# Optimization experiments

Measured on AMD Instinct MI355X. Metric: run time of the kernel, lower is better.

## Reference

```python
import jax, jax.numpy as jnp
import numpy as np

HID = 50  # HIDDEN_SIZE in source


def _lstm_step(x, h, c, W_ih, W_hh, b):
    # PyTorch LSTM cell: gates order i, f, g, o
    gates = x @ W_ih.T + h @ W_hh.T + b  # [B, 4H]
    i, f, g, o = jnp.split(gates, 4, axis=-1)
    i = jax.nn.sigmoid(i)
    f = jax.nn.sigmoid(f)
    g = jnp.tanh(g)
    o = jax.nn.sigmoid(o)
    c = f * c + i * g
    h = o * jnp.tanh(c)
    return h, c


def setup_inputs() -> dict:
    key = jax.random.key(0)
    ks = jax.random.split(key, 11)
    B, S = 2048, 512
    H, I, O = HID, 1, 1
    s = 1.0 / np.sqrt(H)
    u = lambda k, shp: jax.random.uniform(k, shp, jnp.float32, -s, s)
    return {
        "source": jax.random.normal(ks[0], (B, S, I), jnp.float32),
        "enc_W_ih": u(ks[1], (4 * H, I)),
        "enc_W_hh": u(ks[2], (4 * H, H)),
        "enc_b_ih": u(ks[3], (4 * H,)),
        "enc_b_hh": u(ks[4], (4 * H,)),
        "dec_W_ih": u(ks[5], (4 * H, O)),
        "dec_W_hh": u(ks[6], (4 * H, H)),
        "dec_b_ih": u(ks[7], (4 * H,)),
        "dec_b_hh": u(ks[8], (4 * H,)),
        "fc_W": u(ks[9], (O, H)),
        "fc_b": u(ks[10], (O,)),
        "target_len": 256,
    }


def reference(source, enc_W_ih, enc_W_hh, enc_b_ih, enc_b_hh,
              dec_W_ih, dec_W_hh, dec_b_ih, dec_b_hh, fc_W, fc_b,
              target_len):
    B = source.shape[0]
    H = enc_W_hh.shape[1]
    dt = source.dtype
    h0 = jnp.zeros((B, H), dt)
    c0 = jnp.zeros((B, H), dt)

    enc_b = enc_b_ih + enc_b_hh

    def enc_step(carry, x_t):
        h, c = carry
        h, c = _lstm_step(x_t, h, c, enc_W_ih, enc_W_hh, enc_b)
        return (h, c), None

    # scan over time: [S, B, 1]
    (h, c), _ = jax.lax.scan(enc_step, (h0, c0), jnp.swapaxes(source, 0, 1))

    dec_b = dec_b_ih + dec_b_hh
    x0 = jnp.zeros((B, source.shape[2]), dt)  # decoder_input = zeros

    def dec_step(carry, _):
        x, h, c = carry
        h, c = _lstm_step(x, h, c, dec_W_ih, dec_W_hh, dec_b)
        y = h @ fc_W.T + fc_b  # [B, 1]
        return (y, h, c), y  # feed output back as next input

    _, ys = jax.lax.scan(dec_step, (x0, h, c), None, length=target_len)
    return jnp.swapaxes(ys, 0, 1)  # [B, target_len, 1]
```

## Files before the change

### kernel.cpp

```cpp
#include <hip/hip_runtime.h>


#define HID 50
#define SEQ 512
#define TGT 256
#define MB  4
#define L2E 1.44269504088896341f

typedef __attribute__((ext_vector_type(8))) short short8;
typedef __attribute__((ext_vector_type(4))) float f32x4;

__device__ __forceinline__ unsigned short f2bf(float f) {
    unsigned u = __float_as_uint(f);
    return (unsigned short)((u + 0x7fffu + ((u >> 16) & 1u)) >> 16);
}
__device__ __forceinline__ float bf2f(unsigned short b) {
    return __uint_as_float(((unsigned)b) << 16);
}
__device__ __forceinline__ float sigm2(float a) {
    return __builtin_amdgcn_rcpf(1.0f + __builtin_amdgcn_exp2f(-a));
}
__device__ __forceinline__ float tanhc(float c) {
    return fmaf(2.0f,
        __builtin_amdgcn_rcpf(1.0f + __builtin_amdgcn_exp2f(-2.0f * L2E * c)),
        -1.0f);
}

#define MFMA(A, B, C) __builtin_amdgcn_mfma_f32_16x16x32_bf16((A), (B), (C), 0, 0, 0)

#define HB(s, kt, qg) ((((s) * 2 + (kt)) * 4 + (qg)) * 32)
#define HFSZ (2 * 2 * 4 * 32)

#define GCOREX(XK, POSTX, HIN, HOUT)                                   \
    float hv;                                                          \
    {                                                                  \
        const short* hin_ = (HIN);                                     \
        short8 a00 = *(const short8*)(hin_ + HB(0, 0, kg) + bsel * 8); \
        short8 a10 = *(const short8*)(hin_ + HB(0, 1, kg) + bsel * 8); \
        short8 a01 = *(const short8*)(hin_ + HB(1, 0, kg) + bsel * 8); \
        short8 a11 = *(const short8*)(hin_ + HB(1, 1, kg) + bsel * 8); \
        float i0, i1, i2, i3;                                          \
        if (POSTX) {                                                   \
            i0 = bb[0]; i1 = bb[1]; i2 = bb[2]; i3 = bb[3];            \
        } else {                                                       \
            i0 = fmaf(wx[0], (XK), bb[0]);                             \
            i1 = fmaf(wx[1], (XK), bb[1]);                             \
            i2 = fmaf(wx[2], (XK), bb[2]);                             \
            i3 = fmaf(wx[3], (XK), bb[3]);                             \
        }                                                              \
        f32x4 cA0 = {i0, i0, i0, i0};                                  \
        f32x4 cA1 = {i1, i1, i1, i1};                                  \
        f32x4 cA2 = {i2, i2, i2, i2};                                  \
        f32x4 cA3 = {i3, i3, i3, i3};                                  \
        f32x4 cB0 = {0.0f, 0.0f, 0.0f, 0.0f};                          \
        f32x4 cB1 = cB0, cB2 = cB0, cB3 = cB0;                         \
        cA0 = MFMA(a00, Bf[0][0][0], cA0);                             \
        cB0 = MFMA(a10, Bf[0][1][0], cB0);                             \
        cA1 = MFMA(a00, Bf[1][0][0], cA1);                             \
        cB1 = MFMA(a10, Bf[1][1][0], cB1);                             \
        cA2 = MFMA(a00, Bf[2][0][0], cA2);                             \
        cB2 = MFMA(a10, Bf[2][1][0], cB2);                             \
        cA3 = MFMA(a00, Bf[3][0][0], cA3);                             \
        cB3 = MFMA(a10, Bf[3][1][0], cB3);                             \
        cA0 = MFMA(a00, Bf[0][0][1], cA0);                             \
        cB0 = MFMA(a10, Bf[0][1][1], cB0);                             \
        cA1 = MFMA(a00, Bf[1][0][1], cA1);                             \
        cB1 = MFMA(a10, Bf[1][1][1], cB1);                             \
        cA2 = MFMA(a00, Bf[2][0][1], cA2);                             \
        cB2 = MFMA(a10, Bf[2][1][1], cB2);                             \
        cA3 = MFMA(a00, Bf[3][0][1], cA3);                             \
        cB3 = MFMA(a10, Bf[3][1][1], cB3);                             \
        cA0 = MFMA(a01, Bf[0][0][0], cA0);                             \
        cB0 = MFMA(a11, Bf[0][1][0], cB0);                             \
        cA1 = MFMA(a01, Bf[1][0][0], cA1);                             \
        cB1 = MFMA(a11, Bf[1][1][0], cB1);                             \
        cA2 = MFMA(a01, Bf[2][0][0], cA2);                             \
        cB2 = MFMA(a11, Bf[2][1][0], cB2);                             \
        cA3 = MFMA(a01, Bf[3][0][0], cA3);                             \
        cB3 = MFMA(a11, Bf[3][1][0], cB3);                             \
        float s0 = cA0[0] + cB0[0];                                    \
        float s1 = cA1[0] + cB1[0];                                    \
        float s2 = cA2[0] + cB2[0];                                    \
        float s3 = cA3[0] + cB3[0];                                    \
        if (POSTX) {                                                   \
            s0 = fmaf(wx[0], xc, s0);                                  \
            s1 = fmaf(wx[1], xc, s1);                                  \
            s2 = fmaf(wx[2], xc, s2);                                  \
            s3 = fmaf(wx[3], xc, s3);                                  \
        }                                                              \
        float vi = sigm2(s0);                                          \
        float vf = sigm2(s1);                                          \
        float vg = fmaf(2.0f, sigm2(s2), -1.0f);                       \
        float vo = sigm2(s3);                                          \
        cc = fmaf(vf, cc, vi * vg);                                    \
        hv = vo * tanhc(cc);                                           \
        unsigned short q0 = f2bf(hv);                                  \
        unsigned short q1 = f2bf(hv - bf2f(q0));                       \
        short* ho_ = (HOUT);                                           \
        ho_[wr0] = (short)q0;                                          \
        ho_[wr1] = (short)q1;                                          \
    }

#define DSTEP(T, HIN, HOUT, PB)                                        \
    {                                                                  \
        GCOREX(0.0f, 1, HIN, HOUT)                                     \
        float p = fcw * hv;                                            \
        p += __shfl_xor(p, 1, 64);                                     \
        p += __shfl_xor(p, 2, 64);                                     \
        p += __shfl_xor(p, 4, 64);                                     \
        p += __shfl_xor(p, 8, 64);                                     \
        if (nl == 0) (PB)[kg * 4 + w] = p;                             \
        __syncthreads();                                               \
        f32x4 s_ = *(const f32x4*)&(PB)[kg * 4];                       \
        float y = s_[0] + s_[1] + s_[2] + s_[3] + fb;                  \
        if (w == 0 && nl == 0) out[(size_t)(b0 + kg) * TGT + (T)] = y; \
        xc = y;                                                        \
    }

extern "C" __global__ void __launch_bounds__(256, 2)
seq2seq_kernel(const float* __restrict__ src,
               const float* __restrict__ eWih, const float* __restrict__ eWhh,
               const float* __restrict__ eBih, const float* __restrict__ eBhh,
               const float* __restrict__ dWih, const float* __restrict__ dWhh,
               const float* __restrict__ dBih, const float* __restrict__ dBhh,
               const float* __restrict__ fcW, const float* __restrict__ fcB,
               float* __restrict__ out) {
    const int tid  = threadIdx.x;
    const int lane = tid & 63;
    const int w    = tid >> 6;
    const int nl   = lane & 15;
    const int kg   = lane >> 4;
    const int bsel = nl >> 2;
    const int un   = 16 * w + nl;
    const int b0   = blockIdx.x * MB;
    const int ukt  = un >> 5, uqg = (un >> 3) & 3, uj = un & 7;
    const int wr0  = HB(0, ukt, uqg) + kg * 8 + uj;
    const int wr1  = HB(1, ukt, uqg) + kg * 8 + uj;

    __shared__ __align__(16) short hfA[HFSZ], hfB[HFSZ];
    __shared__ __align__(16) float srcT[SEQ * MB];
    __shared__ __align__(16) float pbA[16], pbB[16];

    for (int i = tid; i < HFSZ; i += 256) { hfA[i] = 0; hfB[i] = 0; }
    for (int i = tid; i < SEQ * MB; i += 256) {
        int e = i >> 9, t = i & 511;
        srcT[t * MB + e] = src[(size_t)(b0 + e) * SEQ + t];
    }

    short8 Bf[4][2][2];
    float bb[4], wx[4];
    float cc = 0.0f;
    float xc = 0.0f;

    auto loadW = [&](const float* Wih, const float* Whh,
                     const float* Bih, const float* Bhh) {
#pragma unroll
        for (int g = 0; g < 4; ++g) {
            const float sc = (g == 2) ? 2.0f * L2E : L2E;
            const bool nv  = (un < HID);
            const int row  = g * HID + (nv ? un : 0);
            bb[g] = nv ? (Bih[row] + Bhh[row]) * sc : 0.0f;
            wx[g] = nv ? Wih[row] * sc : 0.0f;
#pragma unroll
            for (int kt = 0; kt < 2; ++kt) {
                short8 s0, s1;
#pragma unroll
                for (int j = 0; j < 8; ++j) {
                    int kk = kt * 32 + kg * 8 + j;
                    float wv = (nv && kk < HID)
                             ? Whh[(size_t)row * HID + kk] * sc : 0.0f;
                    unsigned short h0 = f2bf(wv);
                    unsigned short h1 = f2bf(wv - bf2f(h0));
                    s0[j] = (short)h0; s1[j] = (short)h1;
                }
                Bf[g][kt][0] = s0; Bf[g][kt][1] = s1;
            }
        }
    };

    loadW(eWih, eWhh, eBih, eBhh);
    __syncthreads();
    for (int t = 0; t < SEQ; t += 2) {
        { GCOREX(srcT[t * MB + kg], 0, hfA, hfB) }
        __syncthreads();
        { GCOREX(srcT[(t + 1) * MB + kg], 0, hfB, hfA) }
        __syncthreads();
    }

    loadW(dWih, dWhh, dBih, dBhh);
    const float fcw = (un < HID) ? fcW[un] : 0.0f;
    const float fb  = fcB[0];
    for (int t = 0; t < TGT; t += 2) {
        DSTEP(t,     hfA, hfB, pbA)
        DSTEP(t + 1, hfB, hfA, pbB)
    }
}

extern "C" void kernel_launch(void* const* d_in, const int* in_sizes, int n_in,
                              void* d_out, int out_size, void* d_ws, size_t ws_size,
                              hipStream_t stream) {
    const float* src  = (const float*)d_in[0];
    const float* eWih = (const float*)d_in[1];
    const float* eWhh = (const float*)d_in[2];
    const float* eBih = (const float*)d_in[3];
    const float* eBhh = (const float*)d_in[4];
    const float* dWih = (const float*)d_in[5];
    const float* dWhh = (const float*)d_in[6];
    const float* dBih = (const float*)d_in[7];
    const float* dBhh = (const float*)d_in[8];
    const float* fcW  = (const float*)d_in[9];
    const float* fcB  = (const float*)d_in[10];
    float* out = (float*)d_out;

    const int B = in_sizes[0] / SEQ;
    seq2seq_kernel<<<B / MB, 256, 0, stream>>>(src, eWih, eWhh, eBih, eBhh,
                                               dWih, dWhh, dBih, dBhh,
                                               fcW, fcB, out);
}
```

Baseline: 531.7 us.

## Interleave two independent batch groups per block to share barriers and add ILP

Each block now handles 8 batch rows as two independent 4-row LSTM recurrences, each with its own h buffers, cell state and decoder feedback, interleaved inside one step. The two groups share each __syncthreads and the decoder reduction barrier. This is meant to hide MFMA and transcendental latency in the serial recurrence and halve barriers per batch row. In exchange the grid is halved, launch bounds drop to one block per CU, and register and LDS use per block roughly doubles.

```diff
diff --git a/kernel.cpp b/kernel.cpp
--- a/kernel.cpp
+++ b/kernel.cpp
@@ -4,7 +4,7 @@
 #define HID 50
 #define SEQ 512
 #define TGT 256
-#define MB  4
+#define MB  8
 #define L2E 1.44269504088896341f
 
 typedef __attribute__((ext_vector_type(8))) short short8;
@@ -31,8 +31,7 @@
 #define HB(s, kt, qg) ((((s) * 2 + (kt)) * 4 + (qg)) * 32)
 #define HFSZ (2 * 2 * 4 * 32)
 
-#define GCOREX(XK, POSTX, HIN, HOUT)                                   \
-    float hv;                                                          \
+#define GCOREX(XK, POSTX, XC, CC, HV, HIN, HOUT)                       \
     {                                                                  \
         const short* hin_ = (HIN);                                     \
         short8 a00 = *(const short8*)(hin_ + HB(0, 0, kg) + bsel * 8); \
@@ -83,41 +82,52 @@
         float s2 = cA2[0] + cB2[0];                                    \
         float s3 = cA3[0] + cB3[0];                                    \
         if (POSTX) {                                                   \
-            s0 = fmaf(wx[0], xc, s0);                                  \
-            s1 = fmaf(wx[1], xc, s1);                                  \
-            s2 = fmaf(wx[2], xc, s2);                                  \
-            s3 = fmaf(wx[3], xc, s3);                                  \
+            s0 = fmaf(wx[0], (XC), s0);                                \
+            s1 = fmaf(wx[1], (XC), s1);                                \
+            s2 = fmaf(wx[2], (XC), s2);                                \
+            s3 = fmaf(wx[3], (XC), s3);                                \
         }                                                              \
         float vi = sigm2(s0);                                          \
         float vf = sigm2(s1);                                          \
         float vg = fmaf(2.0f, sigm2(s2), -1.0f);                       \
         float vo = sigm2(s3);                                          \
-        cc = fmaf(vf, cc, vi * vg);                                    \
-        hv = vo * tanhc(cc);                                           \
-        unsigned short q0 = f2bf(hv);                                  \
-        unsigned short q1 = f2bf(hv - bf2f(q0));                       \
+        (CC) = fmaf(vf, (CC), vi * vg);                                \
+        (HV) = vo * tanhc(CC);                                         \
+        unsigned short q0 = f2bf(HV);                                  \
+        unsigned short q1 = f2bf((HV) - bf2f(q0));                     \
         short* ho_ = (HOUT);                                           \
         ho_[wr0] = (short)q0;                                          \
         ho_[wr1] = (short)q1;                                          \
     }
 
-#define DSTEP(T, HIN, HOUT, PB)                                        \
+#define DSTEP2(T, HIN0, HOUT0, HIN1, HOUT1, PB0, PB1)                  \
     {                                                                  \
-        GCOREX(0.0f, 1, HIN, HOUT)                                     \
-        float p = fcw * hv;                                            \
-        p += __shfl_xor(p, 1, 64);                                     \
-        p += __shfl_xor(p, 2, 64);                                     \
-        p += __shfl_xor(p, 4, 64);                                     \
-        p += __shfl_xor(p, 8, 64);                                     \
-        if (nl == 0) (PB)[kg * 4 + w] = p;                             \
+        GCOREX(0.0f, 1, xc0, cc0, hv0, HIN0, HOUT0)                    \
+        GCOREX(0.0f, 1, xc1, cc1, hv1, HIN1, HOUT1)                    \
+        float p0 = fcw * hv0;                                          \
+        float p1 = fcw * hv1;                                          \
+        p0 += __shfl_xor(p0, 1, 64);                                   \
+        p1 += __shfl_xor(p1, 1, 64);                                   \
+        p0 += __shfl_xor(p0, 2, 64);                                   \
+        p1 += __shfl_xor(p1, 2, 64);                                   \
+        p0 += __shfl_xor(p0, 4, 64);                                   \
+        p1 += __shfl_xor(p1, 4, 64);                                   \
+        p0 += __shfl_xor(p0, 8, 64);                                   \
+        p1 += __shfl_xor(p1, 8, 64);                                   \
+        if (nl == 0) { (PB0)[kg * 4 + w] = p0; (PB1)[kg * 4 + w] = p1; }\
         __syncthreads();                                               \
-        f32x4 s_ = *(const f32x4*)&(PB)[kg * 4];                       \
-        float y = s_[0] + s_[1] + s_[2] + s_[3] + fb;                  \
-        if (w == 0 && nl == 0) out[(size_t)(b0 + kg) * TGT + (T)] = y; \
-        xc = y;                                                        \
-    }
-
-extern "C" __global__ void __launch_bounds__(256, 2)
+        f32x4 u0 = *(const f32x4*)&(PB0)[kg * 4];                      \
+        f32x4 u1 = *(const f32x4*)&(PB1)[kg * 4];                      \
+        float y0 = u0[0] + u0[1] + u0[2] + u0[3] + fb;                 \
+        float y1 = u1[0] + u1[1] + u1[2] + u1[3] + fb;                 \
+        if (w == 0 && nl == 0) {                                       \
+            out[(size_t)(b0 + kg) * TGT + (T)]     = y0;               \
+            out[(size_t)(b0 + 4 + kg) * TGT + (T)] = y1;               \
+        }                                                              \
+        xc0 = y0; xc1 = y1;                                            \
+    }
+
+extern "C" __global__ void __launch_bounds__(256, 1)
 seq2seq_kernel(const float* __restrict__ src,
                const float* __restrict__ eWih, const float* __restrict__ eWhh,
                const float* __restrict__ eBih, const float* __restrict__ eBhh,
@@ -137,11 +147,14 @@
     const int wr0  = HB(0, ukt, uqg) + kg * 8 + uj;
     const int wr1  = HB(1, ukt, uqg) + kg * 8 + uj;
 
-    __shared__ __align__(16) short hfA[HFSZ], hfB[HFSZ];
+    __shared__ __align__(16) short hA0[HFSZ], hB0[HFSZ];
+    __shared__ __align__(16) short hA1[HFSZ], hB1[HFSZ];
     __shared__ __align__(16) float srcT[SEQ * MB];
-    __shared__ __align__(16) float pbA[16], pbB[16];
-
-    for (int i = tid; i < HFSZ; i += 256) { hfA[i] = 0; hfB[i] = 0; }
+    __shared__ __align__(16) float pbA0[16], pbB0[16], pbA1[16], pbB1[16];
+
+    for (int i = tid; i < HFSZ; i += 256) {
+        hA0[i] = 0; hB0[i] = 0; hA1[i] = 0; hB1[i] = 0;
+    }
     for (int i = tid; i < SEQ * MB; i += 256) {
         int e = i >> 9, t = i & 511;
         srcT[t * MB + e] = src[(size_t)(b0 + e) * SEQ + t];
@@ -149,8 +162,9 @@
 
     short8 Bf[4][2][2];
     float bb[4], wx[4];
-    float cc = 0.0f;
-    float xc = 0.0f;
+    float cc0 = 0.0f, cc1 = 0.0f;
+    float hv0, hv1;
+    float xc0 = 0.0f, xc1 = 0.0f;
 
     auto loadW = [&](const float* Wih, const float* Whh,
                      const float* Bih, const float* Bhh) {
@@ -170,8 +184,7 @@
                     float wv = (nv && kk < HID)
                              ? Whh[(size_t)row * HID + kk] * sc : 0.0f;
                     unsigned short h0 = f2bf(wv);
-                    unsigned short h1 = f2bf(wv - bf2f(h0));
-                    s0[j] = (short)h0; s1[j] = (short)h1;
+                    s0[j] = (short)h0; s1[j] = (short)f2bf(wv - bf2f(h0));
                 }
                 Bf[g][kt][0] = s0; Bf[g][kt][1] = s1;
             }
@@ -181,9 +194,11 @@
     loadW(eWih, eWhh, eBih, eBhh);
     __syncthreads();
     for (int t = 0; t < SEQ; t += 2) {
-        { GCOREX(srcT[t * MB + kg], 0, hfA, hfB) }
+        GCOREX(srcT[t * MB + kg],     0, 0.0f, cc0, hv0, hA0, hB0)
+        GCOREX(srcT[t * MB + 4 + kg], 0, 0.0f, cc1, hv1, hA1, hB1)
         __syncthreads();
-        { GCOREX(srcT[(t + 1) * MB + kg], 0, hfB, hfA) }
+        GCOREX(srcT[(t + 1) * MB + kg],     0, 0.0f, cc0, hv0, hB0, hA0)
+        GCOREX(srcT[(t + 1) * MB + 4 + kg], 0, 0.0f, cc1, hv1, hB1, hA1)
         __syncthreads();
     }
 
@@ -191,8 +206,8 @@
     const float fcw = (un < HID) ? fcW[un] : 0.0f;
     const float fb  = fcB[0];
     for (int t = 0; t < TGT; t += 2) {
-        DSTEP(t,     hfA, hfB, pbA)
-        DSTEP(t + 1, hfB, hfA, pbB)
+        DSTEP2(t,     hA0, hB0, hA1, hB1, pbA0, pbA1)
+        DSTEP2(t + 1, hB0, hA0, hB1, hA1, pbB0, pbB1)
     }
 }
 
```

New measurement: 664.5 us. 25.0% more time.
